# Kernel optimization log

Measured on AMD Instinct MI355X. Metric: run time of the kernel, lower is better.

Reference implementation:

```python
import jax, jax.numpy as jnp
import numpy as np

B, S, D, H = 2, 2048, 1024, 16
DK = D // H


def setup_inputs() -> dict:
    key = jax.random.key(0)
    ks = jax.random.split(key, 8)
    scale = 1.0 / np.sqrt(D)
    return {
        "Q": jax.random.normal(ks[0], (B, S, D), jnp.float32),
        "K": jax.random.normal(ks[1], (B, S, D), jnp.float32),
        "V": jax.random.normal(ks[2], (B, S, D), jnp.float32),
        "Wq": jax.random.normal(ks[3], (D, D), jnp.float32) * scale,
        "Wk": jax.random.normal(ks[4], (D, D), jnp.float32) * scale,
        "Wv": jax.random.normal(ks[5], (D, D), jnp.float32) * scale,
        "Wo": jax.random.normal(ks[6], (D, D), jnp.float32) * scale,
        "bo": jax.random.normal(ks[7], (D,), jnp.float32) * 0.01,
    }


def reference(Q, K, V, Wq, Wk, Wv, Wo, bo):
    # Projections: [B,S,D] @ [D,D]
    q = (Q @ Wq).reshape(B, S, H, DK).transpose(0, 2, 1, 3)  # [B,H,S,dk]
    k = (K @ Wk).reshape(B, S, H, DK).transpose(0, 2, 1, 3)
    v = (V @ Wv).reshape(B, S, H, DK).transpose(0, 2, 1, 3)
    scores = jnp.einsum("bhsd,bhtd->bhst", q, k) / jnp.sqrt(jnp.float32(DK))
    # causal mask (masked=True): disallow t > s
    causal = jnp.tril(jnp.ones((S, S), dtype=bool))  # True = keep
    scores = jnp.where(causal[None, None], scores, -jnp.inf)
    attn = jax.nn.softmax(scores, axis=-1)
    out = jnp.einsum("bhst,bhtd->bhsd", attn, v)  # [B,H,S,dk]
    out = out.transpose(0, 2, 1, 3).reshape(B, S, D)
    return out @ Wo + bo
```

## Files before the change

kernel.cpp:

```cpp
#include <hip/hip_runtime.h>
#include <hip/hip_bf16.h>

typedef unsigned short ushort_t;
typedef __attribute__((ext_vector_type(8))) short short8;
typedef __attribute__((ext_vector_type(4))) float f32x4;
typedef __attribute__((ext_vector_type(2))) unsigned int uint2v;

#define B_  2
#define S_  2048
#define D_  1024
#define H_  16
#define DK_ 64

#define NEG_BIG (-1e30f)
#define SCALE2 0.18033688011112042f

__device__ __forceinline__ void async16(const void* g, void* l) {
  __builtin_amdgcn_global_load_lds((const __attribute__((address_space(1))) void*)g,
                                   (__attribute__((address_space(3))) void*)l, 16, 0, 0);
}
__device__ __forceinline__ ushort_t f2bf(float x) {
  __hip_bfloat16 h = __float2bfloat16(x);
  ushort_t u; __builtin_memcpy(&u, &h, 2); return u;
}
__device__ __forceinline__ unsigned int pack_bf2(float lo, float hi) {
  __hip_bfloat162 h2 = __float22bfloat162_rn(make_float2(lo, hi));
  unsigned int u; __builtin_memcpy(&u, &h2, 4); return u;
}

__global__ __launch_bounds__(256) void convert_bf16(const float* Q, const float* K,
                                                    const float* V, ushort_t* qb,
                                                    ushort_t* kb, ushort_t* vb) {
  const float* src = (blockIdx.z == 0) ? Q : (blockIdx.z == 1) ? K : V;
  ushort_t* dst = (blockIdx.z == 0) ? qb : (blockIdx.z == 1) ? kb : vb;
  size_t i = ((size_t)blockIdx.x * 256 + threadIdx.x) * 8;
  f32x4 a = *(const f32x4*)(src + i);
  f32x4 b = *(const f32x4*)(src + i + 4);
  short8 p;
  p[0] = (short)f2bf(a[0]); p[1] = (short)f2bf(a[1]);
  p[2] = (short)f2bf(a[2]); p[3] = (short)f2bf(a[3]);
  p[4] = (short)f2bf(b[0]); p[5] = (short)f2bf(b[1]);
  p[6] = (short)f2bf(b[2]); p[7] = (short)f2bf(b[3]);
  *(short8*)(dst + i) = p;
}

__global__ __launch_bounds__(256) void transpose_w(const float* W0, const float* W1,
                                                   const float* W2, const float* W3,
                                                   ushort_t* out) {
  __shared__ float tile[64][65];
  const float* W = (blockIdx.z == 0) ? W0 : (blockIdx.z == 1) ? W1
                 : (blockIdx.z == 2) ? W2 : W3;
  ushort_t* O = out + (size_t)blockIdx.z * D_ * D_;
  int tx = threadIdx.x & 63, ty = threadIdx.x >> 6;
  int r0 = blockIdx.y * 64, c0 = blockIdx.x * 64;
  for (int i = 0; i < 16; i++) {
    int r = ty + i * 4;
    tile[r][tx] = W[(size_t)(r0 + r) * D_ + c0 + tx];
  }
  __syncthreads();
  for (int i = 0; i < 16; i++) {
    int r = ty + i * 4;
    O[(size_t)(c0 + r) * D_ + r0 + tx] = f2bf(tile[tx][r]);
  }
}

__device__ __forceinline__ void gemm128(const ushort_t* A, const ushort_t* Bt,
                                        int bm, int bn, f32x4 acc[4][4],
                                        ushort_t* As, ushort_t* Bs,
                                        int lane, int w, int wm, int wn) {
  int l16 = lane & 15, quad = lane >> 4;
  for (int mi = 0; mi < 4; mi++)
    for (int ni = 0; ni < 4; ni++) acc[mi][ni] = (f32x4){0.f, 0.f, 0.f, 0.f};
  int arow = lane >> 2, aseg = (lane & 3) * 8;
  for (int k0 = 0; k0 < D_; k0 += 32) {
    __syncthreads();
    for (int j = 0; j < 2; j++) {
      int rb = w * 32 + j * 16;
      async16(A + (size_t)(bm + rb + arow) * D_ + k0 + aseg, As + rb * 32);
      async16(Bt + (size_t)(bn + rb + arow) * D_ + k0 + aseg, Bs + rb * 32);
    }
    __syncthreads();
    short8 af[4], bfv[4];
    for (int mi = 0; mi < 4; mi++)
      af[mi] = *(const short8*)(As + (wm + mi * 16 + l16) * 32 + quad * 8);
    for (int ni = 0; ni < 4; ni++)
      bfv[ni] = *(const short8*)(Bs + (wn + ni * 16 + l16) * 32 + quad * 8);
    for (int mi = 0; mi < 4; mi++)
      for (int ni = 0; ni < 4; ni++)
        acc[mi][ni] = __builtin_amdgcn_mfma_f32_16x16x32_bf16(af[mi], bfv[ni], acc[mi][ni], 0, 0, 0);
  }
}

__global__ __launch_bounds__(256) void qkv_proj(const ushort_t* qb, const ushort_t* kb,
                                                const ushort_t* vb, const ushort_t* Wt,
                                                ushort_t* qh, ushort_t* kh, ushort_t* vT) {
  __shared__ alignas(16) ushort_t As[128 * 32];
  __shared__ alignas(16) ushort_t Bs[128 * 32];
  int tid = threadIdx.x, lane = tid & 63, w = tid >> 6;
  int wm = (w & 1) * 64, wn = (w >> 1) * 64;
  int bm = blockIdx.y * 128, bn = blockIdx.x * 128;
  int z = blockIdx.z;
  const ushort_t* A = (z == 0) ? qb : (z == 1) ? kb : vb;
  const ushort_t* Bt = Wt + (size_t)z * D_ * D_;
  f32x4 acc[4][4];
  gemm128(A, Bt, bm, bn, acc, As, Bs, lane, w, wm, wn);
  int l16 = lane & 15, quad = lane >> 4;
  float qscale = (z == 0) ? SCALE2 : 1.0f;
  for (int mi = 0; mi < 4; mi++)
    for (int ni = 0; ni < 4; ni++)
      for (int r = 0; r < 4; r++) {
        int row = bm + wm + mi * 16 + quad * 4 + r;
        int col = bn + wn + ni * 16 + l16;
        int b = row >> 11, s = row & (S_ - 1);
        int h = col >> 6, dk = col & 63;
        float v = acc[mi][ni][r] * qscale;
        if (z == 2)
          vT[((size_t)(b * H_ + h) * DK_ + dk) * S_ + s] = f2bf(v);
        else {
          ushort_t* dst = (z == 0) ? qh : kh;
          dst[((size_t)(b * H_ + h) * S_ + s) * DK_ + dk] = f2bf(v);
        }
      }
}

__global__ __launch_bounds__(256) void out_proj(const ushort_t* A, const ushort_t* Wt,
                                                const float* bias, float* C) {
  __shared__ alignas(16) ushort_t As[128 * 32];
  __shared__ alignas(16) ushort_t Bs[128 * 32];
  int tid = threadIdx.x, lane = tid & 63, w = tid >> 6;
  int wm = (w & 1) * 64, wn = (w >> 1) * 64;
  int bm = blockIdx.y * 128, bn = blockIdx.x * 128;
  f32x4 acc[4][4];
  gemm128(A, Wt, bm, bn, acc, As, Bs, lane, w, wm, wn);
  int l16 = lane & 15, quad = lane >> 4;
  for (int ni = 0; ni < 4; ni++) {
    int col = bn + wn + ni * 16 + l16;
    float bv = bias[col];
    for (int mi = 0; mi < 4; mi++)
      for (int r = 0; r < 4; r++) {
        int row = bm + wm + mi * 16 + quad * 4 + r;
        C[(size_t)row * D_ + col] = acc[mi][ni][r] + bv;
      }
  }
}

__global__ __launch_bounds__(256) void flash_attn(const ushort_t* qh, const ushort_t* kh,
                                                  const ushort_t* vT, ushort_t* outO) {
  __shared__ alignas(16) ushort_t Ks[2][64 * 64];
  __shared__ alignas(16) ushort_t Vs[2][64 * 64];
  __shared__ alignas(16) ushort_t Ps[4][32 * 72];
  int tid = threadIdx.x, lane = tid & 63, w = tid >> 6;
  int l16 = lane & 15, quad = lane >> 4;
  int qi = 15 - (blockIdx.x >> 5);
  int bh = blockIdx.x & 31;
  int qs = qi * 128;
  int wrow = w * 32;
  const ushort_t* qb = qh + (size_t)bh * S_ * DK_;
  const ushort_t* kb = kh + (size_t)bh * S_ * DK_;
  const ushort_t* vb = vT + (size_t)bh * DK_ * S_;

  short8 qf[2][2];
  for (int mi = 0; mi < 2; mi++) {
    const ushort_t* qp = qb + (size_t)(qs + wrow + mi * 16 + l16) * DK_;
    qf[mi][0] = *(const short8*)(qp + quad * 8);
    qf[mi][1] = *(const short8*)(qp + 32 + quad * 8);
  }
  float m_r[2], l_r[2];
  f32x4 o[2][4];
  for (int mi = 0; mi < 2; mi++) { m_r[mi] = NEG_BIG; l_r[mi] = 0.f; }
  for (int mi = 0; mi < 2; mi++)
    for (int f = 0; f < 4; f++) o[mi][f] = (f32x4){0.f, 0.f, 0.f, 0.f};
  ushort_t* ps = Ps[w];
  int srow = lane >> 3;
  int lseg8 = ((lane & 7) ^ srow) * 8;
  int swz = l16 & 7;

  int nt = (qs >> 6) + 2;
  int buf = 0;
  for (int j = 0; j < 2; j++) {
    int rb = w * 16 + j * 8;
    async16(kb + (size_t)(rb + srow) * DK_ + lseg8, Ks[0] + rb * 64);
    async16(vb + (size_t)(rb + srow) * S_ + lseg8, Vs[0] + rb * 64);
  }
  for (int it = 0; it < nt; it++) {
    int t0 = it << 6;
    __syncthreads();
    if (it + 1 < nt) {
      int t1 = t0 + 64, nb = buf ^ 1;
      for (int j = 0; j < 2; j++) {
        int rb = w * 16 + j * 8;
        async16(kb + (size_t)(t1 + rb + srow) * DK_ + lseg8, Ks[nb] + rb * 64);
        async16(vb + (size_t)(rb + srow) * S_ + t1 + lseg8, Vs[nb] + rb * 64);
      }
    }
    if (t0 <= qs + wrow + 31) {
      const ushort_t* Kb = Ks[buf];
      const ushort_t* Vb = Vs[buf];
      f32x4 sf[2][4];
      for (int mi = 0; mi < 2; mi++)
        for (int f = 0; f < 4; f++) sf[mi][f] = (f32x4){0.f, 0.f, 0.f, 0.f};
      for (int st = 0; st < 2; st++) {
        short8 kfr[4];
        for (int f = 0; f < 4; f++)
          kfr[f] = *(const short8*)(Kb + (f * 16 + l16) * 64 + (((st * 4 + quad) ^ swz) * 8));
        for (int mi = 0; mi < 2; mi++)
          for (int f = 0; f < 4; f++)
            sf[mi][f] = __builtin_amdgcn_mfma_f32_16x16x32_bf16(kfr[f], qf[mi][st], sf[mi][f], 0, 0, 0);
      }
      if (t0 + 63 > qs + wrow) {
        for (int mi = 0; mi < 2; mi++) {
          int s = qs + wrow + mi * 16 + l16;
          for (int f = 0; f < 4; f++) {
            int tb = t0 + f * 16 + quad * 4;
            for (int r = 0; r < 4; r++)
              if (tb + r > s) sf[mi][f][r] = NEG_BIG;
          }
        }
      }
      for (int mi = 0; mi < 2; mi++) {
        float mx = sf[mi][0][0];
        for (int f = 0; f < 4; f++)
          for (int r = 0; r < 4; r++) mx = fmaxf(mx, sf[mi][f][r]);
        mx = fmaxf(mx, __shfl_xor(mx, 16, 64));
        mx = fmaxf(mx, __shfl_xor(mx, 32, 64));
        float mnew = fmaxf(m_r[mi], mx);
        float sum = 0.f;
        for (int f = 0; f < 4; f++)
          for (int r = 0; r < 4; r++) {
            float p = exp2f(sf[mi][f][r] - mnew);
            sf[mi][f][r] = p;
            sum += p;
          }
        sum += __shfl_xor(sum, 16, 64);
        sum += __shfl_xor(sum, 32, 64);
        float alpha = exp2f(m_r[mi] - mnew);
        l_r[mi] = l_r[mi] * alpha + sum;
        m_r[mi] = mnew;
        for (int f = 0; f < 4; f++)
          for (int r = 0; r < 4; r++) o[mi][f][r] *= alpha;
        for (int f = 0; f < 4; f++) {
          uint2v pk;
          pk.x = pack_bf2(sf[mi][f][0], sf[mi][f][1]);
          pk.y = pack_bf2(sf[mi][f][2], sf[mi][f][3]);
          *(uint2v*)(ps + (mi * 16 + l16) * 72 + f * 16 + quad * 4) = pk;
        }
      }
      asm volatile("s_waitcnt lgkmcnt(0)" ::: "memory");
      for (int st = 0; st < 2; st++) {
        short8 vfr[4];
        for (int f = 0; f < 4; f++)
          vfr[f] = *(const short8*)(Vb + (f * 16 + l16) * 64 + (((st * 4 + quad) ^ swz) * 8));
        for (int mi = 0; mi < 2; mi++) {
          short8 pf = *(const short8*)(ps + (mi * 16 + l16) * 72 + st * 32 + quad * 8);
          for (int f = 0; f < 4; f++)
            o[mi][f] = __builtin_amdgcn_mfma_f32_16x16x32_bf16(vfr[f], pf, o[mi][f], 0, 0, 0);
        }
      }
    }
    buf ^= 1;
  }
  int b = bh >> 4, h = bh & 15;
  for (int mi = 0; mi < 2; mi++) {
    float inv = 1.0f / l_r[mi];
    int s = qs + wrow + mi * 16 + l16;
    ushort_t* op = outO + (size_t)(b * S_ + s) * D_ + h * DK_;
    for (int f = 0; f < 4; f++) {
      uint2v pk;
      pk.x = pack_bf2(o[mi][f][0] * inv, o[mi][f][1] * inv);
      pk.y = pack_bf2(o[mi][f][2] * inv, o[mi][f][3] * inv);
      *(uint2v*)(op + f * 16 + quad * 4) = pk;
    }
  }
}

extern "C" void kernel_launch(void* const* d_in, const int* in_sizes, int n_in,
                              void* d_out, int out_size, void* d_ws, size_t ws_size,
                              hipStream_t stream) {
  const float* Q  = (const float*)d_in[0];
  const float* K  = (const float*)d_in[1];
  const float* V  = (const float*)d_in[2];
  const float* Wq = (const float*)d_in[3];
  const float* Wk = (const float*)d_in[4];
  const float* Wv = (const float*)d_in[5];
  const float* Wo = (const float*)d_in[6];
  const float* bo = (const float*)d_in[7];
  ushort_t* ws = (ushort_t*)d_ws;
  ushort_t* Wt = ws;
  ushort_t* qb = ws + ((size_t)4 << 20);
  ushort_t* kb = ws + ((size_t)8 << 20);
  ushort_t* vb = ws + ((size_t)12 << 20);
  ushort_t* qh = ws + ((size_t)16 << 20);
  ushort_t* kh = ws + ((size_t)20 << 20);
  ushort_t* vT = ws + ((size_t)24 << 20);
  ushort_t* aO = qb;

  convert_bf16<<<dim3(2048, 1, 3), 256, 0, stream>>>(Q, K, V, qb, kb, vb);
  transpose_w<<<dim3(16, 16, 4), 256, 0, stream>>>(Wq, Wk, Wv, Wo, Wt);
  qkv_proj<<<dim3(8, 32, 3), 256, 0, stream>>>(qb, kb, vb, Wt, qh, kh, vT);
  flash_attn<<<512, 256, 0, stream>>>(qh, kh, vT, aO);
  out_proj<<<dim3(8, 32, 1), 256, 0, stream>>>(aO, Wt + ((size_t)3 << 20), bo, (float*)d_out);
}
```

Baseline: 249.4 us.

## Pair complementary causal query tiles per block and shrink per-warp rows

```diff
diff --git a/kernel.cpp b/kernel.cpp
--- a/kernel.cpp
+++ b/kernel.cpp
@@ -148,126 +148,114 @@
                                                   const ushort_t* vT, ushort_t* outO) {
   __shared__ alignas(16) ushort_t Ks[2][64 * 64];
   __shared__ alignas(16) ushort_t Vs[2][64 * 64];
-  __shared__ alignas(16) ushort_t Ps[4][32 * 72];
+  __shared__ alignas(16) ushort_t Ps[4][16 * 72];
   int tid = threadIdx.x, lane = tid & 63, w = tid >> 6;
   int l16 = lane & 15, quad = lane >> 4;
-  int qi = 15 - (blockIdx.x >> 5);
+  int p = blockIdx.x >> 5;
   int bh = blockIdx.x & 31;
-  int qs = qi * 128;
-  int wrow = w * 32;
+  int b = bh >> 4, h = bh & 15;
   const ushort_t* qb = qh + (size_t)bh * S_ * DK_;
   const ushort_t* kb = kh + (size_t)bh * S_ * DK_;
   const ushort_t* vb = vT + (size_t)bh * DK_ * S_;
-
-  short8 qf[2][2];
-  for (int mi = 0; mi < 2; mi++) {
-    const ushort_t* qp = qb + (size_t)(qs + wrow + mi * 16 + l16) * DK_;
-    qf[mi][0] = *(const short8*)(qp + quad * 8);
-    qf[mi][1] = *(const short8*)(qp + 32 + quad * 8);
-  }
-  float m_r[2], l_r[2];
-  f32x4 o[2][4];
-  for (int mi = 0; mi < 2; mi++) { m_r[mi] = NEG_BIG; l_r[mi] = 0.f; }
-  for (int mi = 0; mi < 2; mi++)
-    for (int f = 0; f < 4; f++) o[mi][f] = (f32x4){0.f, 0.f, 0.f, 0.f};
   ushort_t* ps = Ps[w];
   int srow = lane >> 3;
   int lseg8 = ((lane & 7) ^ srow) * 8;
   int swz = l16 & 7;
-
-  int nt = (qs >> 6) + 2;
+  int wrow = w * 16;
+
   int buf = 0;
-  for (int j = 0; j < 2; j++) {
-    int rb = w * 16 + j * 8;
-    async16(kb + (size_t)(rb + srow) * DK_ + lseg8, Ks[0] + rb * 64);
-    async16(vb + (size_t)(rb + srow) * S_ + lseg8, Vs[0] + rb * 64);
-  }
-  for (int it = 0; it < nt; it++) {
-    int t0 = it << 6;
-    __syncthreads();
-    if (it + 1 < nt) {
-      int t1 = t0 + 64, nb = buf ^ 1;
-      for (int j = 0; j < 2; j++) {
-        int rb = w * 16 + j * 8;
-        async16(kb + (size_t)(t1 + rb + srow) * DK_ + lseg8, Ks[nb] + rb * 64);
-        async16(vb + (size_t)(rb + srow) * S_ + t1 + lseg8, Vs[nb] + rb * 64);
-      }
-    }
-    if (t0 <= qs + wrow + 31) {
+  for (int half = 0; half < 2; half++) {
+    int j = half ? p : (31 - p);
+    int qs = j * 64;
+    int nt = j + 1;
+    short8 qf[2];
+    {
+      const ushort_t* qp = qb + (size_t)(qs + wrow + l16) * DK_;
+      qf[0] = *(const short8*)(qp + quad * 8);
+      qf[1] = *(const short8*)(qp + 32 + quad * 8);
+    }
+    float m_r = NEG_BIG, l_r = 0.f;
+    f32x4 o[4];
+    for (int f = 0; f < 4; f++) o[f] = (f32x4){0.f, 0.f, 0.f, 0.f};
+    for (int jj = 0; jj < 2; jj++) {
+      int rb = w * 16 + jj * 8;
+      async16(kb + (size_t)(rb + srow) * DK_ + lseg8, Ks[buf] + rb * 64);
+      async16(vb + (size_t)(rb + srow) * S_ + lseg8, Vs[buf] + rb * 64);
+    }
+    for (int it = 0; it < nt; it++) {
+      int t0 = it << 6;
+      __syncthreads();
+      if (it + 1 < nt) {
+        int t1 = t0 + 64, nb = buf ^ 1;
+        for (int jj = 0; jj < 2; jj++) {
+          int rb = w * 16 + jj * 8;
+          async16(kb + (size_t)(t1 + rb + srow) * DK_ + lseg8, Ks[nb] + rb * 64);
+          async16(vb + (size_t)(rb + srow) * S_ + t1 + lseg8, Vs[nb] + rb * 64);
+        }
+      }
       const ushort_t* Kb = Ks[buf];
       const ushort_t* Vb = Vs[buf];
-      f32x4 sf[2][4];
-      for (int mi = 0; mi < 2; mi++)
-        for (int f = 0; f < 4; f++) sf[mi][f] = (f32x4){0.f, 0.f, 0.f, 0.f};
+      f32x4 sf[4];
+      for (int f = 0; f < 4; f++) sf[f] = (f32x4){0.f, 0.f, 0.f, 0.f};
       for (int st = 0; st < 2; st++) {
         short8 kfr[4];
         for (int f = 0; f < 4; f++)
           kfr[f] = *(const short8*)(Kb + (f * 16 + l16) * 64 + (((st * 4 + quad) ^ swz) * 8));
-        for (int mi = 0; mi < 2; mi++)
-          for (int f = 0; f < 4; f++)
-            sf[mi][f] = __builtin_amdgcn_mfma_f32_16x16x32_bf16(kfr[f], qf[mi][st], sf[mi][f], 0, 0, 0);
-      }
-      if (t0 + 63 > qs + wrow) {
-        for (int mi = 0; mi < 2; mi++) {
-          int s = qs + wrow + mi * 16 + l16;
-          for (int f = 0; f < 4; f++) {
-            int tb = t0 + f * 16 + quad * 4;
-            for (int r = 0; r < 4; r++)
-              if (tb + r > s) sf[mi][f][r] = NEG_BIG;
-          }
-        }
-      }
-      for (int mi = 0; mi < 2; mi++) {
-        float mx = sf[mi][0][0];
-        for (int f = 0; f < 4; f++)
-          for (int r = 0; r < 4; r++) mx = fmaxf(mx, sf[mi][f][r]);
-        mx = fmaxf(mx, __shfl_xor(mx, 16, 64));
-        mx = fmaxf(mx, __shfl_xor(mx, 32, 64));
-        float mnew = fmaxf(m_r[mi], mx);
-        float sum = 0.f;
-        for (int f = 0; f < 4; f++)
-          for (int r = 0; r < 4; r++) {
-            float p = exp2f(sf[mi][f][r] - mnew);
-            sf[mi][f][r] = p;
-            sum += p;
-          }
-        sum += __shfl_xor(sum, 16, 64);
-        sum += __shfl_xor(sum, 32, 64);
-        float alpha = exp2f(m_r[mi] - mnew);
-        l_r[mi] = l_r[mi] * alpha + sum;
-        m_r[mi] = mnew;
-        for (int f = 0; f < 4; f++)
-          for (int r = 0; r < 4; r++) o[mi][f][r] *= alpha;
+        for (int f = 0; f < 4; f++)
+          sf[f] = __builtin_amdgcn_mfma_f32_16x16x32_bf16(kfr[f], qf[st], sf[f], 0, 0, 0);
+      }
+      if (it == nt - 1) {
+        int s = qs + wrow + l16;
         for (int f = 0; f < 4; f++) {
-          uint2v pk;
-          pk.x = pack_bf2(sf[mi][f][0], sf[mi][f][1]);
-          pk.y = pack_bf2(sf[mi][f][2], sf[mi][f][3]);
-          *(uint2v*)(ps + (mi * 16 + l16) * 72 + f * 16 + quad * 4) = pk;
-        }
+          int tb = t0 + f * 16 + quad * 4;
+          for (int r = 0; r < 4; r++)
+            if (tb + r > s) sf[f][r] = NEG_BIG;
+        }
+      }
+      float mx = sf[0][0];
+      for (int f = 0; f < 4; f++)
+        for (int r = 0; r < 4; r++) mx = fmaxf(mx, sf[f][r]);
+      mx = fmaxf(mx, __shfl_xor(mx, 16, 64));
+      mx = fmaxf(mx, __shfl_xor(mx, 32, 64));
+      float mnew = fmaxf(m_r, mx);
+      float sum = 0.f;
+      for (int f = 0; f < 4; f++)
+        for (int r = 0; r < 4; r++) {
+          float pv = exp2f(sf[f][r] - mnew);
+          sf[f][r] = pv;
+          sum += pv;
+        }
+      sum += __shfl_xor(sum, 16, 64);
+      sum += __shfl_xor(sum, 32, 64);
+      float alpha = exp2f(m_r - mnew);
+      l_r = l_r * alpha + sum;
+      m_r = mnew;
+      for (int f = 0; f < 4; f++)
+        for (int r = 0; r < 4; r++) o[f][r] *= alpha;
+      for (int f = 0; f < 4; f++) {
+        uint2v pk;
+        pk.x = pack_bf2(sf[f][0], sf[f][1]);
+        pk.y = pack_bf2(sf[f][2], sf[f][3]);
+        *(uint2v*)(ps + l16 * 72 + f * 16 + quad * 4) = pk;
       }
       asm volatile("s_waitcnt lgkmcnt(0)" ::: "memory");
       for (int st = 0; st < 2; st++) {
         short8 vfr[4];
         for (int f = 0; f < 4; f++)
           vfr[f] = *(const short8*)(Vb + (f * 16 + l16) * 64 + (((st * 4 + quad) ^ swz) * 8));
-        for (int mi = 0; mi < 2; mi++) {
-          short8 pf = *(const short8*)(ps + (mi * 16 + l16) * 72 + st * 32 + quad * 8);
-          for (int f = 0; f < 4; f++)
-            o[mi][f] = __builtin_amdgcn_mfma_f32_16x16x32_bf16(vfr[f], pf, o[mi][f], 0, 0, 0);
-        }
-      }
-    }
-    buf ^= 1;
-  }
-  int b = bh >> 4, h = bh & 15;
-  for (int mi = 0; mi < 2; mi++) {
-    float inv = 1.0f / l_r[mi];
-    int s = qs + wrow + mi * 16 + l16;
+        short8 pf = *(const short8*)(ps + l16 * 72 + st * 32 + quad * 8);
+        for (int f = 0; f < 4; f++)
+          o[f] = __builtin_amdgcn_mfma_f32_16x16x32_bf16(vfr[f], pf, o[f], 0, 0, 0);
+      }
+      buf ^= 1;
+    }
+    float inv = 1.0f / l_r;
+    int s = qs + wrow + l16;
     ushort_t* op = outO + (size_t)(b * S_ + s) * D_ + h * DK_;
     for (int f = 0; f < 4; f++) {
       uint2v pk;
-      pk.x = pack_bf2(o[mi][f][0] * inv, o[mi][f][1] * inv);
-      pk.y = pack_bf2(o[mi][f][2] * inv, o[mi][f][3] * inv);
+      pk.x = pack_bf2(o[f][0] * inv, o[f][1] * inv);
+      pk.y = pack_bf2(o[f][2] * inv, o[f][3] * inv);
       *(uint2v*)(op + f * 16 + quad * 4) = pk;
     }
   }
```

Result: faster. 234.7 us (-5.9%).
